# Performance work log

Hardware: AMD Instinct MI355X
Metric: run time of the kernel (lower is better)

## Reference

```python
import jax, jax.numpy as jnp
import numpy as np

N = 50000   # nodes
E = 800000  # edges
F_IN, H, C, G = 128, 96, 16, 128  # features, hidden, classes, graphs


def gelu(x):
    return jax.nn.gelu(x, approximate=False)  # torch F.gelu default (erf)


def gcn_conv(x, W, b, src, dst, dis):
    # PyG GCNConv improved=True: A_hat = A + 2I, out = D^-1/2 A_hat D^-1/2 (x W) + b
    xw = x @ W                                   # [N, out]
    norm = dis[src] * dis[dst]                   # [E]
    msg = norm[:, None] * xw[src]                # gather + scale
    out = jax.ops.segment_sum(msg, dst, num_segments=N)
    out = out + (2.0 * dis * dis)[:, None] * xw  # self-loop with weight 2
    return out + b


def setup_inputs() -> dict:
    key = jax.random.key(0)
    ks = jax.random.split(key, 12)
    x = jax.random.normal(ks[0], (N, F_IN), dtype=jnp.float32)
    edge_index = jax.random.randint(ks[1], (2, E), 0, N, dtype=jnp.int64)
    batch = jnp.sort(jax.random.randint(ks[2], (N,), 0, G, dtype=jnp.int64))
    s = lambda fan_in: 1.0 / np.sqrt(fan_in)
    W0 = jax.random.uniform(ks[3], (F_IN, H), jnp.float32, -s(F_IN), s(F_IN))
    b0 = jnp.zeros((H,), jnp.float32)
    W1 = jax.random.uniform(ks[4], (H, H), jnp.float32, -s(H), s(H))
    b1 = jnp.zeros((H,), jnp.float32)
    W2 = jax.random.uniform(ks[5], (H, H), jnp.float32, -s(H), s(H))
    b2 = jnp.zeros((H,), jnp.float32)
    Wc1 = jax.random.uniform(ks[6], (2 * H, H), jnp.float32, -s(2 * H), s(2 * H))
    bc1 = jax.random.uniform(ks[7], (H,), jnp.float32, -s(2 * H), s(2 * H))
    Wc2 = jax.random.uniform(ks[8], (H, C), jnp.float32, -s(H), s(H))
    bc2 = jax.random.uniform(ks[9], (C,), jnp.float32, -s(H), s(H))
    return {"x": x, "edge_index": edge_index, "batch": batch,
            "W0": W0, "b0": b0, "W1": W1, "b1": b1, "W2": W2, "b2": b2,
            "Wc1": Wc1, "bc1": bc1, "Wc2": Wc2, "bc2": bc2}


def reference(x, edge_index, batch, W0, b0, W1, b1, W2, b2, Wc1, bc1, Wc2, bc2):
    src, dst = edge_index[0], edge_index[1]
    # degrees including self-loop weight 2 (improved=True)
    deg = jax.ops.segment_sum(jnp.ones((E,), x.dtype), dst, num_segments=N) + 2.0
    dis = jax.lax.rsqrt(deg)
    # layer 0: GCNConv(F_IN -> H)
    h = gcn_conv(x, W0, b0, src, dst, dis)
    # residual GCNConv layers (dropout is identity at inference)
    h = h + gcn_conv(gelu(h), W1, b1, src, dst, dis)
    h = h + gcn_conv(gelu(h), W2, b2, src, dst, dis)
    h = gelu(h)
    # global mean + max pooling per graph
    cnt = jax.ops.segment_sum(jnp.ones((N,), h.dtype), batch, num_segments=G)
    mean_p = jax.ops.segment_sum(h, batch, num_segments=G) / cnt[:, None]
    max_p = jax.ops.segment_max(h, batch, num_segments=G)
    p = jnp.concatenate([mean_p, max_p], axis=1)  # [G, 2H]
    p = p @ Wc1 + bc1
    p = gelu(p)
    return p @ Wc2 + bc2
```

## Files before the change

### kernel.cpp

```cpp
#include <hip/hip_runtime.h>
#include <hip/hip_bf16.h>

#define DEVINL __device__ __forceinline__

constexpr int N = 50000;
constexpr int E = 800000;
constexpr int F_IN = 128;
constexpr int H = 96;
constexpr int C = 16;
constexpr int G = 128;
constexpr int S = 8;
constexpr int ELLW = 64;

constexpr int OFF_W0  = 0;
constexpr int OFF_W1  = OFF_W0 + F_IN * H;
constexpr int OFF_W2  = OFF_W1 + H * H;
constexpr int OFF_WC1 = OFF_W2 + H * H;
constexpr int OFF_WC2 = OFF_WC1 + 2 * H * H;
constexpr int OFF_B0  = OFF_WC2 + H * C;
constexpr int OFF_B1  = OFF_B0 + H;
constexpr int OFF_B2  = OFF_B1 + H;
constexpr int OFF_BC1 = OFF_B2 + H;
constexpr int OFF_BC2 = OFF_BC1 + H;
constexpr int WF_TOT  = OFF_BC2 + C;

constexpr int CVB   = (WF_TOT + 255) / 256;
constexpr int GEMB  = (N + 31) / 32;
constexpr int SCATB = (E / 2 + 127) / 128;

DEVINL float gelu_f(float x) {
    return 0.5f * x * (1.0f + erff(x * 0.70710678118654752440f));
}

DEVINL int detect_eidx_i64(const int* e) {
    int z = 0;
#pragma unroll
    for (int i = 1; i < 16; i += 2) z |= e[i];
    return z == 0;
}
DEVINL int detect_batch_i64(const int* a) {
    int z = 0;
    for (int i = 20001; i < 20032; i += 2) z |= a[i];
    return z == 0;
}
DEVINL int detect_x_f32(const unsigned short* xu) {
    int bad = 0;
    for (int i = 0; i < 128; i += 2) { int ex = (xu[i] >> 7) & 0xFF; if (ex >= 132) bad = 1; }
    return bad;
}

DEVINL unsigned pk(float a, float b) {
    __hip_bfloat16 ha = __float2bfloat16(a), hb = __float2bfloat16(b);
    unsigned short ua = *(unsigned short*)&ha, ub = *(unsigned short*)&hb;
    return (unsigned)ua | ((unsigned)ub << 16);
}
DEVINL float lo16(unsigned u) { return __uint_as_float(u << 16); }
DEVINL float hi16(unsigned u) { return __uint_as_float(u & 0xffff0000u); }

DEVINL float disv(int c) { return rsqrtf((float)c + 2.0f); }

__global__ void k_prep(const void* W0, const void* W1, const void* W2,
                       const void* Wc1, const void* Wc2,
                       const void* b0, const void* b1, const void* b2,
                       const void* bc1, const void* bc2,
                       const void* x, float* __restrict__ wf, int* __restrict__ cnt) {
    int i = blockIdx.x * 256 + threadIdx.x;
    if (i < N) cnt[i] = 0;
    if (i >= WF_TOT) return;
    int f32 = detect_x_f32((const unsigned short*)x);
    const void* src; int j;
    if      (i < OFF_W1)  { src = W0;  j = i - OFF_W0; }
    else if (i < OFF_W2)  { src = W1;  j = i - OFF_W1; }
    else if (i < OFF_WC1) { src = W2;  j = i - OFF_W2; }
    else if (i < OFF_WC2) { src = Wc1; j = i - OFF_WC1; }
    else if (i < OFF_B0)  { src = Wc2; j = i - OFF_WC2; }
    else if (i < OFF_B1)  { src = b0;  j = i - OFF_B0; }
    else if (i < OFF_B2)  { src = b1;  j = i - OFF_B1; }
    else if (i < OFF_BC1) { src = b2;  j = i - OFF_B2; }
    else if (i < OFF_BC2) { src = bc1; j = i - OFF_BC1; }
    else                  { src = bc2; j = i - OFF_BC2; }
    wf[i] = f32 ? ((const float*)src)[j]
                : __bfloat162float(((const __hip_bfloat16*)src)[j]);
}

template<int K, int KC, bool RAW_IN, bool GELU_IN, bool SCALE_OUT>
DEVINL void gemm_tile(const void* __restrict__ inp, const float* __restrict__ Wf,
                      const int* __restrict__ cnt,
                      int xf32, unsigned* __restrict__ out, int bid, int t) {
    constexpr int R = 32;
    constexpr int NC = K / KC;
    __shared__ __align__(16) float xs[KC][R + 4];
    __shared__ __align__(16) float wsh[KC * 96];
    const int r0 = bid * R;
    const int ty = t >> 4;
    const int tx = t & 15;

    float acc[4][6];
#pragma unroll
    for (int i = 0; i < 4; ++i)
#pragma unroll
        for (int j = 0; j < 6; ++j) acc[i][j] = 0.f;

    for (int c = 0; c < NC; ++c) {
        if (c) __syncthreads();
        for (int idx = t * 4; idx < KC * 96; idx += 128 * 4)
            *(float4*)&wsh[idx] = *(const float4*)&Wf[c * KC * 96 + idx];
        if (RAW_IN && !xf32) {
            for (int idx = t; idx < R * KC; idx += 128) {
                int r = idx / KC, kk = idx - r * KC;
                int row = r0 + r, k = c * KC + kk;
                float v = 0.f;
                if (row < N) v = __bfloat162float(((const __hip_bfloat16*)inp)[(size_t)row * K + k]);
                xs[kk][r] = v;
            }
        } else {
            constexpr int KC4 = KC / 4;
            for (int idx = t; idx < R * KC4; idx += 128) {
                int r = idx / KC4, k4 = (idx - r * KC4) * 4;
                int row = r0 + r, k = c * KC + k4;
                float4 v = make_float4(0.f, 0.f, 0.f, 0.f);
                if (row < N) v = *(const float4*)((const float*)inp + (size_t)row * K + k);
                if (GELU_IN) { v.x = gelu_f(v.x); v.y = gelu_f(v.y); v.z = gelu_f(v.z); v.w = gelu_f(v.w); }
                xs[k4 + 0][r] = v.x; xs[k4 + 1][r] = v.y; xs[k4 + 2][r] = v.z; xs[k4 + 3][r] = v.w;
            }
        }
        __syncthreads();

#pragma unroll 4
        for (int kk = 0; kk < KC; ++kk) {
            float4 av = *(const float4*)&xs[kk][ty * 4];
            float2 b0 = *(const float2*)&wsh[kk * 96 + tx * 6];
            float2 b1 = *(const float2*)&wsh[kk * 96 + tx * 6 + 2];
            float2 b2 = *(const float2*)&wsh[kk * 96 + tx * 6 + 4];
            float a[4] = {av.x, av.y, av.z, av.w};
            float b[6] = {b0.x, b0.y, b1.x, b1.y, b2.x, b2.y};
#pragma unroll
            for (int i = 0; i < 4; ++i)
#pragma unroll
                for (int j = 0; j < 6; ++j)
                    acc[i][j] = fmaf(a[i], b[j], acc[i][j]);
        }
    }

#pragma unroll
    for (int i = 0; i < 4; ++i) {
        int row = r0 + ty * 4 + i;
        if (row < N) {
            float d = SCALE_OUT ? disv(cnt[row]) : 1.0f;
            unsigned* o = out + (size_t)row * 48 + tx * 3;
            o[0] = pk(d * acc[i][0], d * acc[i][1]);
            o[1] = pk(d * acc[i][2], d * acc[i][3]);
            o[2] = pk(d * acc[i][4], d * acc[i][5]);
        }
    }
}

__global__ __launch_bounds__(128) void k_sg(const void* __restrict__ x,
                                            const float* __restrict__ Wf,
                                            const int* __restrict__ eidx,
                                            int* __restrict__ cnt, int* __restrict__ ell,
                                            unsigned* __restrict__ outZ) {
    int b = blockIdx.x, t = threadIdx.x;
    if (b % 3 == 0) {
        int gb = b / 3;
        if (gb >= GEMB) return;
        int xf32 = detect_x_f32((const unsigned short*)x);
        gemm_tile<F_IN, 32, true, false, false>(x, Wf, nullptr, xf32, outZ, gb, t);
        return;
    }
    int sb = (b / 3) * 2 + (b % 3) - 1;
    if (sb >= SCATB) return;
    int t2 = sb * 128 + t;
    int e = 2 * t2;
    if (e >= E) return;
    int i64 = detect_eidx_i64(eidx);
    int s0, s1, d0, d1;
    if (i64) {
        int4 sp = *(const int4*)(eidx + 4 * t2);
        int4 dp = *(const int4*)(eidx + 2 * E + 4 * t2);
        s0 = sp.x; s1 = sp.z; d0 = dp.x; d1 = dp.z;
    } else {
        int2 sp = *(const int2*)(eidx + 2 * t2);
        int2 dp = *(const int2*)(eidx + E + 2 * t2);
        s0 = sp.x; s1 = sp.y; d0 = dp.x; d1 = dp.y;
    }
    int p0 = atomicAdd(&cnt[d0], 1);
    if (p0 < ELLW) ell[d0 * ELLW + p0] = s0;
    if (e + 1 < E) {
        int p1 = atomicAdd(&cnt[d1], 1);
        if (p1 < ELLW) ell[d1 * ELLW + p1] = s1;
    }
}

template<int K, int KC, bool GELU_IN>
__global__ __launch_bounds__(128) void k_gemm(const float* __restrict__ inp,
                                              const float* __restrict__ Wf,
                                              const int* __restrict__ cnt,
                                              unsigned* __restrict__ out) {
    gemm_tile<K, KC, false, GELU_IN, true>(inp, Wf, cnt, 1, out, blockIdx.x, threadIdx.x);
}

template<bool PRESCALED>
__global__ __launch_bounds__(256) void k_aggr(const unsigned* __restrict__ xw, const float* res,
                                              const int* __restrict__ ell, const int* __restrict__ cnt,
                                              const float* __restrict__ bias, float* __restrict__ out) {
    int wid = threadIdx.x >> 6, lane = threadIdx.x & 63;
    int n = blockIdx.x * 4 + wid;
    if (n >= N) return;
    int cn = cnt[n];
    int e0 = n * ELLW;
    int e1 = e0 + min(cn, ELLW);
    int slot = lane / 12;
    int li = lane - slot * 12;
    int cp = li * 4;
    float4 A0 = make_float4(0.f, 0.f, 0.f, 0.f);
    float4 A1 = make_float4(0.f, 0.f, 0.f, 0.f);
    int eb = (slot < 5) ? (e0 + slot) : e1;
    for (; eb + 10 < e1; eb += 15) {
        int s0 = ell[eb];
        int s1 = ell[eb + 5];
        int s2 = ell[eb + 10];
        uint4 u0 = *(const uint4*)(xw + (size_t)s0 * 48 + cp);
        uint4 u1 = *(const uint4*)(xw + (size_t)s1 * 48 + cp);
        uint4 u2 = *(const uint4*)(xw + (size_t)s2 * 48 + cp);
        if (PRESCALED) {
            A0.x += lo16(u0.x) + lo16(u1.x) + lo16(u2.x);
            A0.y += hi16(u0.x) + hi16(u1.x) + hi16(u2.x);
            A0.z += lo16(u0.y) + lo16(u1.y) + lo16(u2.y);
            A0.w += hi16(u0.y) + hi16(u1.y) + hi16(u2.y);
            A1.x += lo16(u0.z) + lo16(u1.z) + lo16(u2.z);
            A1.y += hi16(u0.z) + hi16(u1.z) + hi16(u2.z);
            A1.z += lo16(u0.w) + lo16(u1.w) + lo16(u2.w);
            A1.w += hi16(u0.w) + hi16(u1.w) + hi16(u2.w);
        } else {
            float w0 = disv(cnt[s0]), w1 = disv(cnt[s1]), w2 = disv(cnt[s2]);
            A0.x = fmaf(w0, lo16(u0.x), A0.x); A0.y = fmaf(w0, hi16(u0.x), A0.y);
            A0.z = fmaf(w0, lo16(u0.y), A0.z); A0.w = fmaf(w0, hi16(u0.y), A0.w);
            A1.x = fmaf(w0, lo16(u0.z), A1.x); A1.y = fmaf(w0, hi16(u0.z), A1.y);
            A1.z = fmaf(w0, lo16(u0.w), A1.z); A1.w = fmaf(w0, hi16(u0.w), A1.w);
            A0.x = fmaf(w1, lo16(u1.x), A0.x); A0.y = fmaf(w1, hi16(u1.x), A0.y);
            A0.z = fmaf(w1, lo16(u1.y), A0.z); A0.w = fmaf(w1, hi16(u1.y), A0.w);
            A1.x = fmaf(w1, lo16(u1.z), A1.x); A1.y = fmaf(w1, hi16(u1.z), A1.y);
            A1.z = fmaf(w1, lo16(u1.w), A1.z); A1.w = fmaf(w1, hi16(u1.w), A1.w);
            A0.x = fmaf(w2, lo16(u2.x), A0.x); A0.y = fmaf(w2, hi16(u2.x), A0.y);
            A0.z = fmaf(w2, lo16(u2.y), A0.z); A0.w = fmaf(w2, hi16(u2.y), A0.w);
            A1.x = fmaf(w2, lo16(u2.z), A1.x); A1.y = fmaf(w2, hi16(u2.z), A1.y);
            A1.z = fmaf(w2, lo16(u2.w), A1.z); A1.w = fmaf(w2, hi16(u2.w), A1.w);
        }
    }
    for (; eb < e1; eb += 5) {
        int s = ell[eb];
        uint4 u = *(const uint4*)(xw + (size_t)s * 48 + cp);
        if (PRESCALED) {
            A0.x += lo16(u.x); A0.y += hi16(u.x); A0.z += lo16(u.y); A0.w += hi16(u.y);
            A1.x += lo16(u.z); A1.y += hi16(u.z); A1.z += lo16(u.w); A1.w += hi16(u.w);
        } else {
            float w = disv(cnt[s]);
            A0.x = fmaf(w, lo16(u.x), A0.x); A0.y = fmaf(w, hi16(u.x), A0.y);
            A0.z = fmaf(w, lo16(u.y), A0.z); A0.w = fmaf(w, hi16(u.y), A0.w);
            A1.x = fmaf(w, lo16(u.z), A1.x); A1.y = fmaf(w, hi16(u.z), A1.y);
            A1.z = fmaf(w, lo16(u.w), A1.z); A1.w = fmaf(w, hi16(u.w), A1.w);
        }
    }
    {
        float g0, g1, g2, g3;
        g0 = __shfl(A0.x, lane + 12); g1 = __shfl(A0.x, lane + 24); g2 = __shfl(A0.x, lane + 36); g3 = __shfl(A0.x, lane + 48);
        A0.x += g0 + g1 + g2 + g3;
        g0 = __shfl(A0.y, lane + 12); g1 = __shfl(A0.y, lane + 24); g2 = __shfl(A0.y, lane + 36); g3 = __shfl(A0.y, lane + 48);
        A0.y += g0 + g1 + g2 + g3;
        g0 = __shfl(A0.z, lane + 12); g1 = __shfl(A0.z, lane + 24); g2 = __shfl(A0.z, lane + 36); g3 = __shfl(A0.z, lane + 48);
        A0.z += g0 + g1 + g2 + g3;
        g0 = __shfl(A0.w, lane + 12); g1 = __shfl(A0.w, lane + 24); g2 = __shfl(A0.w, lane + 36); g3 = __shfl(A0.w, lane + 48);
        A0.w += g0 + g1 + g2 + g3;
        g0 = __shfl(A1.x, lane + 12); g1 = __shfl(A1.x, lane + 24); g2 = __shfl(A1.x, lane + 36); g3 = __shfl(A1.x, lane + 48);
        A1.x += g0 + g1 + g2 + g3;
        g0 = __shfl(A1.y, lane + 12); g1 = __shfl(A1.y, lane + 24); g2 = __shfl(A1.y, lane + 36); g3 = __shfl(A1.y, lane + 48);
        A1.y += g0 + g1 + g2 + g3;
        g0 = __shfl(A1.z, lane + 12); g1 = __shfl(A1.z, lane + 24); g2 = __shfl(A1.z, lane + 36); g3 = __shfl(A1.z, lane + 48);
        A1.z += g0 + g1 + g2 + g3;
        g0 = __shfl(A1.w, lane + 12); g1 = __shfl(A1.w, lane + 24); g2 = __shfl(A1.w, lane + 36); g3 = __shfl(A1.w, lane + 48);
        A1.w += g0 + g1 + g2 + g3;
    }

    if (lane < 12) {
        float dn = disv(cn);
        float sc = PRESCALED ? (2.f * dn) : (2.f * dn * dn);
        int cl = li * 8;
        uint4 su = *(const uint4*)(xw + (size_t)n * 48 + cp);
        float4 sv0 = make_float4(lo16(su.x), hi16(su.x), lo16(su.y), hi16(su.y));
        float4 sv1 = make_float4(lo16(su.z), hi16(su.z), lo16(su.w), hi16(su.w));
        float4 bv0 = *(const float4*)(bias + cl);
        float4 bv1 = *(const float4*)(bias + cl + 4);
        float4 rv0 = make_float4(0.f, 0.f, 0.f, 0.f);
        float4 rv1 = make_float4(0.f, 0.f, 0.f, 0.f);
        if (res) {
            rv0 = *(const float4*)(res + (size_t)n * 96 + cl);
            rv1 = *(const float4*)(res + (size_t)n * 96 + cl + 4);
        }
        float4 o0, o1;
        o0.x = rv0.x + dn * A0.x + sc * sv0.x + bv0.x;
        o0.y = rv0.y + dn * A0.y + sc * sv0.y + bv0.y;
        o0.z = rv0.z + dn * A0.z + sc * sv0.z + bv0.z;
        o0.w = rv0.w + dn * A0.w + sc * sv0.w + bv0.w;
        o1.x = rv1.x + dn * A1.x + sc * sv1.x + bv1.x;
        o1.y = rv1.y + dn * A1.y + sc * sv1.y + bv1.y;
        o1.z = rv1.z + dn * A1.z + sc * sv1.z + bv1.z;
        o1.w = rv1.w + dn * A1.w + sc * sv1.w + bv1.w;
        *(float4*)(out + (size_t)n * 96 + cl) = o0;
        *(float4*)(out + (size_t)n * 96 + cl + 4) = o1;
    }
}

DEVINL int ld_idx(const int* a, int i64, int i) { return i64 ? a[2 * i] : a[i]; }

DEVINL int lbound_s(const int* a, int i64, int n, int key) {
    int lo = 0, hi = n;
    while (lo < hi) { int m = (lo + hi) >> 1; if (ld_idx(a, i64, m) < key) lo = m + 1; else hi = m; }
    return lo;
}

__global__ __launch_bounds__(128) void k_pool(const float* __restrict__ h, const int* __restrict__ batch,
                                              float* __restrict__ part) {
    int i64 = detect_batch_i64(batch);
    int g = blockIdx.x / S, sch = blockIdx.x % S;
    int lo = lbound_s(batch, i64, N, g), hi = lbound_s(batch, i64, N, g + 1);
    int len = hi - lo;
    int a = lo + (int)(((long long)len * sch) / S);
    int b = lo + (int)(((long long)len * (sch + 1)) / S);
    int t = threadIdx.x;
    if (t < 96) {
        float s0 = 0.f, s1 = 0.f, m0 = -INFINITY, m1 = -INFINITY;
        int n = a;
        for (; n + 1 < b; n += 2) {
            float v0 = gelu_f(h[(size_t)n * 96 + t]);
            float v1 = gelu_f(h[(size_t)(n + 1) * 96 + t]);
            s0 += v0; s1 += v1;
            m0 = fmaxf(m0, v0); m1 = fmaxf(m1, v1);
        }
        if (n < b) {
            float v = gelu_f(h[(size_t)n * 96 + t]);
            s0 += v; m0 = fmaxf(m0, v);
        }
        part[(size_t)blockIdx.x * 192 + t] = s0 + s1;
        part[(size_t)blockIdx.x * 192 + 96 + t] = fmaxf(m0, m1);
    }
}

__global__ __launch_bounds__(128) void k_cls(const float* __restrict__ part, const int* __restrict__ batch,
                                             const void* __restrict__ x,
                                             const float* __restrict__ wf, void* __restrict__ outp) {
    __shared__ float p[192];
    __shared__ float q[96];
    int i64 = detect_batch_i64(batch);
    int g = blockIdx.x, t = threadIdx.x;
    int lo = lbound_s(batch, i64, N, g), hi = lbound_s(batch, i64, N, g + 1);
    float inv = (hi > lo) ? 1.f / (float)(hi - lo) : 0.f;
    if (t < 96) {
        float sum = 0.f, mx = -INFINITY;
        for (int s = 0; s < S; ++s) {
            sum += part[(size_t)(g * S + s) * 192 + t];
            mx = fmaxf(mx, part[(size_t)(g * S + s) * 192 + 96 + t]);
        }
        p[t] = sum * inv;
        p[96 + t] = mx;
    }
    __syncthreads();
    if (t < 96) {
        float acc = wf[OFF_BC1 + t];
        const float* Wc1 = wf + OFF_WC1;
        for (int j = 0; j < 192; ++j)
            acc += p[j] * Wc1[j * 96 + t];
        q[t] = gelu_f(acc);
    }
    __syncthreads();
    if (t < 16) {
        float acc = wf[OFF_BC2 + t];
        const float* Wc2 = wf + OFF_WC2;
        for (int j = 0; j < 96; ++j)
            acc += q[j] * Wc2[j * 16 + t];
        if (detect_x_f32((const unsigned short*)x)) ((float*)outp)[g * 16 + t] = acc;
        else ((__hip_bfloat16*)outp)[g * 16 + t] = __float2bfloat16(acc);
    }
}

extern "C" void kernel_launch(void* const* d_in, const int* in_sizes, int n_in,
                              void* d_out, int out_size, void* d_ws, size_t ws_size,
                              hipStream_t stream) {
    const void* x    = d_in[0];
    const int* eidx  = (const int*)d_in[1];
    const int* batch = (const int*)d_in[2];
    (void)in_sizes; (void)n_in; (void)out_size; (void)ws_size;

    char* w = (char*)d_ws;
    size_t off = 0;
    auto take = [&](size_t bytes) { size_t o = off; off += (bytes + 511) & ~(size_t)511; return o; };
    int*      cnt  = (int*)     (w + take((size_t)N * 4));
    float*    wf   = (float*)   (w + take((size_t)WF_TOT * 4));
    int*      ell  = (int*)     (w + take((size_t)N * ELLW * 4));
    unsigned* bufA = (unsigned*)(w + take((size_t)N * 48 * 4));
    float*    bufH = (float*)   (w + take((size_t)N * 96 * 4));
    float*    part = (float*)   (w + take((size_t)G * S * 192 * 4));

    k_prep<<<CVB, 256, 0, stream>>>(d_in[3], d_in[5], d_in[7], d_in[9], d_in[11],
                                    d_in[4], d_in[6], d_in[8], d_in[10], d_in[12],
                                    x, wf, cnt);
    k_sg<<<3 * GEMB, 128, 0, stream>>>(x, wf + OFF_W0, eidx, cnt, ell, bufA);

    int aggr_grid = (N + 3) / 4;
    k_aggr<false><<<aggr_grid, 256, 0, stream>>>(bufA, nullptr, ell, cnt, wf + OFF_B0, bufH);
    k_gemm<H, 48, true><<<GEMB, 128, 0, stream>>>(bufH, wf + OFF_W1, cnt, bufA);
    k_aggr<true><<<aggr_grid, 256, 0, stream>>>(bufA, bufH, ell, cnt, wf + OFF_B1, bufH);
    k_gemm<H, 48, true><<<GEMB, 128, 0, stream>>>(bufH, wf + OFF_W2, cnt, bufA);
    k_aggr<true><<<aggr_grid, 256, 0, stream>>>(bufA, bufH, ell, cnt, wf + OFF_B2, bufH);

    k_pool<<<G * S, 128, 0, stream>>>(bufH, batch, part);
    k_cls<<<G, 128, 0, stream>>>(part, batch, x, wf, d_out);
}
```

Measured before the change: 356.0 us.

## Build ELL adjacency per node-range with LDS atomics instead of global atomics

```diff
diff --git a/kernel.cpp b/kernel.cpp
--- a/kernel.cpp
+++ b/kernel.cpp
@@ -25,8 +25,10 @@
 constexpr int WF_TOT  = OFF_BC2 + C;
 
 constexpr int CVB   = (WF_TOT + 255) / 256;
+constexpr int EB    = (E / 4 + 255) / 256;
 constexpr int GEMB  = (N + 31) / 32;
-constexpr int SCATB = (E / 2 + 127) / 128;
+constexpr int SCANB = 256;
+constexpr int PB    = (N + SCANB - 1) / SCANB;
 
 DEVINL float gelu_f(float x) {
     return 0.5f * x * (1.0f + erff(x * 0.70710678118654752440f));
@@ -63,9 +65,31 @@
                        const void* Wc1, const void* Wc2,
                        const void* b0, const void* b1, const void* b2,
                        const void* bc1, const void* bc2,
-                       const void* x, float* __restrict__ wf, int* __restrict__ cnt) {
-    int i = blockIdx.x * 256 + threadIdx.x;
-    if (i < N) cnt[i] = 0;
+                       const void* x, const int* __restrict__ eidx,
+                       float* __restrict__ wf,
+                       int* __restrict__ src32, int* __restrict__ dst32) {
+    int b = blockIdx.x, t = threadIdx.x;
+    if (b >= CVB) {
+        int i = (b - CVB) * 256 + t;
+        if (4 * i >= E) return;
+        int i64 = detect_eidx_i64(eidx);
+        int4 s4, d4;
+        if (i64) {
+            int4 a0 = *(const int4*)(eidx + 8 * i);
+            int4 a1 = *(const int4*)(eidx + 8 * i + 4);
+            s4 = make_int4(a0.x, a0.z, a1.x, a1.z);
+            int4 c0 = *(const int4*)(eidx + 2 * E + 8 * i);
+            int4 c1 = *(const int4*)(eidx + 2 * E + 8 * i + 4);
+            d4 = make_int4(c0.x, c0.z, c1.x, c1.z);
+        } else {
+            s4 = *(const int4*)(eidx + 4 * i);
+            d4 = *(const int4*)(eidx + E + 4 * i);
+        }
+        *(int4*)(src32 + 4 * i) = s4;
+        *(int4*)(dst32 + 4 * i) = d4;
+        return;
+    }
+    int i = b * 256 + t;
     if (i >= WF_TOT) return;
     int f32 = detect_x_f32((const unsigned short*)x);
     const void* src; int j;
@@ -157,39 +181,42 @@
 
 __global__ __launch_bounds__(128) void k_sg(const void* __restrict__ x,
                                             const float* __restrict__ Wf,
-                                            const int* __restrict__ eidx,
+                                            const int* __restrict__ src32,
+                                            const int* __restrict__ dst32,
                                             int* __restrict__ cnt, int* __restrict__ ell,
                                             unsigned* __restrict__ outZ) {
     int b = blockIdx.x, t = threadIdx.x;
-    if (b % 3 == 0) {
-        int gb = b / 3;
-        if (gb >= GEMB) return;
-        int xf32 = detect_x_f32((const unsigned short*)x);
-        gemm_tile<F_IN, 32, true, false, false>(x, Wf, nullptr, xf32, outZ, gb, t);
+    int q = b / 7, r = b % 7;
+    if (r == 0 && q < SCANB) {
+        __shared__ int lcnt[PB];
+        int lo = q * PB;
+        int hi = min(lo + PB, N);
+        int nloc = hi - lo;
+        for (int i = t; i < PB; i += 128) lcnt[i] = 0;
+        __syncthreads();
+        for (int base = t * 8; base < E; base += 128 * 8) {
+            int4 a0 = *(const int4*)(dst32 + base);
+            int4 a1 = *(const int4*)(dst32 + base + 4);
+            int ds[8] = {a0.x, a0.y, a0.z, a0.w, a1.x, a1.y, a1.z, a1.w};
+#pragma unroll
+            for (int k = 0; k < 8; ++k) {
+                unsigned rel = (unsigned)(ds[k] - lo);
+                if (rel < (unsigned)nloc) {
+                    int p = atomicAdd(&lcnt[rel], 1);
+                    int s = src32[base + k];
+                    if (p < ELLW) ell[ds[k] * ELLW + p] = s;
+                }
+            }
+        }
+        __syncthreads();
+        for (int i = t; i < nloc; i += 128) cnt[lo + i] = lcnt[i];
         return;
     }
-    int sb = (b / 3) * 2 + (b % 3) - 1;
-    if (sb >= SCATB) return;
-    int t2 = sb * 128 + t;
-    int e = 2 * t2;
-    if (e >= E) return;
-    int i64 = detect_eidx_i64(eidx);
-    int s0, s1, d0, d1;
-    if (i64) {
-        int4 sp = *(const int4*)(eidx + 4 * t2);
-        int4 dp = *(const int4*)(eidx + 2 * E + 4 * t2);
-        s0 = sp.x; s1 = sp.z; d0 = dp.x; d1 = dp.z;
-    } else {
-        int2 sp = *(const int2*)(eidx + 2 * t2);
-        int2 dp = *(const int2*)(eidx + E + 2 * t2);
-        s0 = sp.x; s1 = sp.y; d0 = dp.x; d1 = dp.y;
-    }
-    int p0 = atomicAdd(&cnt[d0], 1);
-    if (p0 < ELLW) ell[d0 * ELLW + p0] = s0;
-    if (e + 1 < E) {
-        int p1 = atomicAdd(&cnt[d1], 1);
-        if (p1 < ELLW) ell[d1 * ELLW + p1] = s1;
-    }
+    int nsb = min(q + (r ? 1 : 0), SCANB);
+    int gb = b - nsb;
+    if (gb >= GEMB) return;
+    int xf32 = detect_x_f32((const unsigned short*)x);
+    gemm_tile<F_IN, 32, true, false, false>(x, Wf, nullptr, xf32, outZ, gb, t);
 }
 
 template<int K, int KC, bool GELU_IN>
@@ -394,17 +421,19 @@
     char* w = (char*)d_ws;
     size_t off = 0;
     auto take = [&](size_t bytes) { size_t o = off; off += (bytes + 511) & ~(size_t)511; return o; };
-    int*      cnt  = (int*)     (w + take((size_t)N * 4));
-    float*    wf   = (float*)   (w + take((size_t)WF_TOT * 4));
-    int*      ell  = (int*)     (w + take((size_t)N * ELLW * 4));
-    unsigned* bufA = (unsigned*)(w + take((size_t)N * 48 * 4));
-    float*    bufH = (float*)   (w + take((size_t)N * 96 * 4));
-    float*    part = (float*)   (w + take((size_t)G * S * 192 * 4));
-
-    k_prep<<<CVB, 256, 0, stream>>>(d_in[3], d_in[5], d_in[7], d_in[9], d_in[11],
-                                    d_in[4], d_in[6], d_in[8], d_in[10], d_in[12],
-                                    x, wf, cnt);
-    k_sg<<<3 * GEMB, 128, 0, stream>>>(x, wf + OFF_W0, eidx, cnt, ell, bufA);
+    int*      cnt   = (int*)     (w + take((size_t)N * 4));
+    float*    wf    = (float*)   (w + take((size_t)WF_TOT * 4));
+    int*      ell   = (int*)     (w + take((size_t)N * ELLW * 4));
+    unsigned* bufA  = (unsigned*)(w + take((size_t)N * 48 * 4));
+    float*    bufH  = (float*)   (w + take((size_t)N * 96 * 4));
+    float*    part  = (float*)   (w + take((size_t)G * S * 192 * 4));
+    int*      src32 = (int*)     (w + take((size_t)E * 4));
+    int*      dst32 = (int*)     (w + take((size_t)E * 4));
+
+    k_prep<<<CVB + EB, 256, 0, stream>>>(d_in[3], d_in[5], d_in[7], d_in[9], d_in[11],
+                                         d_in[4], d_in[6], d_in[8], d_in[10], d_in[12],
+                                         x, eidx, wf, src32, dst32);
+    k_sg<<<GEMB + SCANB, 128, 0, stream>>>(x, wf + OFF_W0, src32, dst32, cnt, ell, bufA);
 
     int aggr_grid = (N + 3) / 4;
     k_aggr<false><<<aggr_grid, 256, 0, stream>>>(bufA, nullptr, ell, cnt, wf + OFF_B0, bufH);
```

After: 829.4 us. 133% more time.
